# Optimization experiments

Hardware: AMD Instinct MI355X
Metric: run time of the kernel (lower is better)

The kernel has to match this reference:

```python
import jax, jax.numpy as jnp
import numpy as np
from jax import lax

B, C_IN, H, W = 16, 64, 64, 64
C_OUT, K, P, NC = 128, 3, 1, 512
PS = C_IN * K * K  # 576 patch feature size


def setup_inputs() -> dict:
    key = jax.random.key(0)
    k0, k1, k2, k3 = jax.random.split(key, 4)
    x = jax.random.normal(k0, (B, C_IN, H, W), jnp.float32)
    cluster_centers = jax.random.normal(k1, (NC, PS), jnp.float32)
    temp = jnp.ones((1,), jnp.float32)
    weight = jax.random.normal(k2, (C_OUT, C_IN, K, K), jnp.float32) * 0.05
    bias = jax.random.normal(k3, (C_OUT,), jnp.float32) * 0.05
    return {"x": x, "cluster_centers": cluster_centers, "temp": temp,
            "weight": weight, "bias": bias}


def _forward(x, cluster_centers, temp, weight, bias):
    Bx, C, Hx, Wx = x.shape
    t = temp.reshape(())  # scalar temperature
    # F.unfold: patches ordered (c, kh, kw) along feature dim -> [B, C*K*K, H, W]
    patches = lax.conv_general_dilated_patches(
        x, (K, K), (1, 1), padding=((P, P), (P, P)))
    L = Hx * Wx  # number of blocks; equals Wx*Wx (H==W, same-padding, stride 1)
    cols = patches.reshape(Bx, PS, L)               # this_patch
    flat = cols.transpose(0, 2, 1).reshape(-1, PS)  # [N, PS] flat_patches
    # torch.cdist (p=2): stable squared-distance expansion, single GEMM
    d2 = (jnp.sum(flat * flat, axis=1, keepdims=True)
          + jnp.sum(cluster_centers * cluster_centers, axis=1)[None, :]
          - 2.0 * (flat @ cluster_centers.T))
    dist = jnp.sqrt(jnp.maximum(d2, 0.0))           # [N, NC]
    soft = jax.nn.softmax(-dist * t, axis=1)        # soft assignments
    transformed = soft @ cluster_centers            # [N, PS]
    final = (t * transformed + flat) / (t + 1.0)
    # Faithful to the original's view_as: raw reshape WITHOUT transposing back
    final = final.reshape(Bx, PS, L)
    # F.fold(output_size=(W*K, W*K), kernel=K, padding=P, stride=K):
    # non-overlapping tiles on padded canvas, then crop P from each side.
    # (b, c, kh, kw, bh, bw) -> (b, c, bh, kh, bw, kw)
    tile = (final.reshape(Bx, C, K, K, Wx, Wx)
                 .transpose(0, 1, 4, 2, 5, 3)
                 .reshape(Bx, C, Wx * K, Wx * K))
    # crop offset P=1 at the top/left; bottom/right of cropped region is zero
    x_refold = jnp.pad(tile[:, :, P:, P:], ((0, 0), (0, 0), (0, P), (0, P)))
    # F.conv2d(..., stride=kernel_size, padding=padding)
    out = lax.conv_general_dilated(
        x_refold, weight, window_strides=(K, K), padding=((P, P), (P, P)),
        dimension_numbers=("NCHW", "OIHW", "NCHW"))
    return out + bias[None, :, None, None]


def reference(x, cluster_centers, temp, weight, bias):
    return _forward(x, cluster_centers, temp, weight, bias)
```

## Files before the change

kernel.cpp:

```cpp
#include <hip/hip_runtime.h>
#include <stdint.h>

typedef __bf16 bf16;
typedef bf16 bf16x2 __attribute__((ext_vector_type(2)));
typedef bf16 bf16x8 __attribute__((ext_vector_type(8)));
typedef float f32x4 __attribute__((ext_vector_type(4)));

static constexpr int B_    = 16;
static constexpr int C_IN  = 64;
static constexpr int H_    = 64;
static constexpr int W_    = 64;
static constexpr int C_OUT = 128;
static constexpr int NC    = 512;
static constexpr int PS    = 576;
static constexpr int L_    = H_ * W_;
static constexpr int NR    = B_ * L_;

#define DEVI __device__ __forceinline__

DEVI void gload_lds16(const void* g, void* l) {
  __builtin_amdgcn_global_load_lds(
      (const __attribute__((address_space(1))) uint32_t*)g,
      (__attribute__((address_space(3))) uint32_t*)l, 16, 0, 0);
}


__global__ void prep_w_kernel(const float* __restrict__ w, bf16* __restrict__ WB,
                              bf16* __restrict__ ccT) {
  int i = blockIdx.x * 256 + threadIdx.x;
  if (i < C_OUT * PS) WB[i] = (bf16)w[i];
  if (i < 64 * NC) ccT[(size_t)PS * NC + i] = (bf16)0.f;
}

__global__ void prep_cc_kernel(const float* __restrict__ cc, bf16* __restrict__ ccB,
                               bf16* __restrict__ ccT, float* __restrict__ cn) {
  int j = blockIdx.x;
  const float* src = cc + (size_t)j * PS;
  float s = 0.f;
  for (int p = threadIdx.x; p < PS; p += 256) {
    float v = src[p];
    bf16 bv = (bf16)v;
    ccB[(size_t)j * PS + p] = bv;
    ccT[(size_t)p * NC + j] = bv;
    float fv = (float)bv;
    s += fv * fv;
  }
  for (int o = 32; o; o >>= 1) s += __shfl_xor(s, o);
  __shared__ float red[4];
  int lane = threadIdx.x & 63, wid = threadIdx.x >> 6;
  if (lane == 0) red[wid] = s;
  __syncthreads();
  if (threadIdx.x == 0) cn[j] = red[0] + red[1] + red[2] + red[3];
}

static constexpr int XS_STRIDE = 66;
static constexpr int XS_PLANE  = 64 * XS_STRIDE;
static constexpr int XS_OFF    = 2;

__global__ void __launch_bounds__(256, 4) patch_kernel(
    const float* __restrict__ x, bf16* __restrict__ flatB,
    float* __restrict__ rn, float* __restrict__ rsum) {
  __shared__ bf16 xs[XS_OFF + 3 * XS_PLANE + 64];
  const int bh = blockIdx.x;
  const int b = bh >> 6, h = bh & 63;
  const size_t bOff = (size_t)b * (C_IN * L_);
#pragma unroll
  for (int it = 0; it < 12; ++it) {
    int idx = threadIdx.x + it * 256;
    int plane = idx >> 10;
    int rem = idx & 1023;
    int c = rem >> 4;
    int f4 = rem & 15;
    int y = h + plane - 1;
    int e = XS_OFF + plane * XS_PLANE + c * XS_STRIDE + f4 * 4;
    bf16x2 lo = {(bf16)0.f, (bf16)0.f}, hi = {(bf16)0.f, (bf16)0.f};
    if ((unsigned)y < 64u) {
      float4 v = *(const float4*)(x + bOff + (size_t)c * L_ + y * 64 + f4 * 4);
      lo = bf16x2{(bf16)v.x, (bf16)v.y};
      hi = bf16x2{(bf16)v.z, (bf16)v.w};
    }
    *(bf16x2*)(xs + e) = lo;
    *(bf16x2*)(xs + e + 2) = hi;
  }
  __syncthreads();

  const int lane = threadIdx.x & 63, wid = threadIdx.x >> 6;
  int eb[8], km[8];
#pragma unroll
  for (int q = 0; q < 8; q++) {
    int p = lane * 8 + q;
    int c = p / 9, r9 = p - c * 9;
    int kh = r9 / 3, kw = r9 - kh * 3;
    eb[q] = kh * XS_PLANE + c * XS_STRIDE + (kw - 1);
    km[q] = kw - 1;
  }
  int ebt[8], kmt[8];
  {
    int pl = (lane & 7) * 8;
#pragma unroll
    for (int q = 0; q < 8; q++) {
      int p = 512 + pl + q;
      int c = p / 9, r9 = p - c * 9;
      int kh = r9 / 3, kw = r9 - kh * 3;
      ebt[q] = kh * XS_PLANE + c * XS_STRIDE + (kw - 1);
      kmt[q] = kw - 1;
    }
  }
  for (int it = 0; it < 16; ++it) {
    int w = wid * 16 + it;
    int row = bh * 64 + w;
    bf16* outp = flatB + (size_t)row * PS;
    float s = 0.f;
    bf16x8 v;
#pragma unroll
    for (int q = 0; q < 8; q++) {
      int xx = w + km[q];
      float fv = ((unsigned)xx < 64u) ? (float)xs[XS_OFF + eb[q] + w] : 0.f;
      v[q] = (bf16)fv;
      s += fv * fv;
    }
    *(bf16x8*)(outp + lane * 8) = v;
    if (lane < 8) {
      bf16x8 v2;
#pragma unroll
      for (int q = 0; q < 8; q++) {
        int xx = w + kmt[q];
        float fv = ((unsigned)xx < 64u) ? (float)xs[XS_OFF + ebt[q] + w] : 0.f;
        v2[q] = (bf16)fv;
        s += fv * fv;
      }
      *(bf16x8*)(outp + 512 + lane * 8) = v2;
    }
    for (int o = 32; o; o >>= 1) s += __shfl_xor(s, o);
    if (lane == 0) { rn[row] = s; rsum[row] = 0.f; }
  }
}

template <int EPI, int GX>
__global__ void __launch_bounds__(256, 5) gemm_nt(
    const bf16* __restrict__ A, int lda, const bf16* __restrict__ Bm, int ldb,
    int M, int N, int Kd,
    const float* __restrict__ e0, const float* __restrict__ e1,
    const float* __restrict__ e2, const bf16* flatB,
    float* outF, bf16* outB, int ldc) {
  const int blk = blockIdx.x;
  const int xcd = blk & 7;
  const int k = blk >> 3;
  const int ypx = (gridDim.x >> 3) / GX;
  const int bx = k % GX;
  const int by = xcd * ypx + k / GX;
  const int m0 = by * 128, n0 = bx * 64;

  __shared__ bf16 As[128 * 64];
  __shared__ bf16 Bs[64 * 64];
  const int tid = threadIdx.x;
  const int lane = tid & 63;
  const int wid = tid >> 6;
  const int wr = wid >> 1, wc = wid & 1;

  const int srow = tid >> 3;
  const int sch = ((tid & 7) ^ (srow & 7)) * 8;
  const bf16* gA = A + (size_t)(m0 + srow) * lda + sch;
  const bf16* gB = Bm + (size_t)(n0 + srow) * ldb + sch;
  bf16* lA = As + tid * 8;
  bf16* lB = Bs + tid * 8;

  const int lrow = lane & 15;
  const int kq = lane >> 4;
  const int axor = lrow & 7;
  const int arow = (wr * 64 + lrow) * 64;
  const int brow = (wc * 32 + lrow) * 64;

  f32x4 acc[4][2];
#pragma unroll
  for (int i = 0; i < 4; i++)
#pragma unroll
    for (int j = 0; j < 2; j++) acc[i][j] = f32x4{0.f, 0.f, 0.f, 0.f};

  const int nk = Kd >> 6;
  for (int kt = 0; kt < nk; ++kt) {
    __syncthreads();
    const bf16* ga = gA + kt * 64;
    const bf16* gb = gB + kt * 64;
#pragma unroll
    for (int q = 0; q < 4; ++q)
      gload_lds16(ga + (size_t)(q * 32) * lda, lA + q * 2048);
#pragma unroll
    for (int q = 0; q < 2; ++q)
      gload_lds16(gb + (size_t)(q * 32) * ldb, lB + q * 2048);
    __syncthreads();
#pragma unroll
    for (int h = 0; h < 2; ++h) {
      const int cs = ((h * 4 + kq) ^ axor) * 8;
      bf16x8 af[4], bfr[2];
#pragma unroll
      for (int i = 0; i < 4; i++) af[i] = *(const bf16x8*)(As + arow + i * 1024 + cs);
#pragma unroll
      for (int j = 0; j < 2; j++) bfr[j] = *(const bf16x8*)(Bs + brow + j * 1024 + cs);
#pragma unroll
      for (int i = 0; i < 4; i++)
#pragma unroll
        for (int j = 0; j < 2; j++)
          acc[i][j] = __builtin_amdgcn_mfma_f32_16x16x32_bf16(af[i], bfr[j], acc[i][j], 0, 0, 0);
    }
  }

  const int rb = m0 + wr * 64 + kq * 4;
  const int cb = n0 + wc * 32 + lrow;
  if constexpr (EPI == 1) {
    float t = e2[0];
#pragma unroll
    for (int i = 0; i < 4; i++) {
      float rowsum[4] = {0.f, 0.f, 0.f, 0.f};
#pragma unroll
      for (int j = 0; j < 2; j++) {
        int col = cb + j * 16;
        float cnv = e1[col];
#pragma unroll
        for (int r = 0; r < 4; r++) {
          int row = rb + i * 16 + r;
          float d2 = e0[row] + cnv - 2.f * acc[i][j][r];
          float e = __expf(-t * sqrtf(fmaxf(d2, 0.f)));
          outB[(size_t)row * ldc + col] = (bf16)e;
          rowsum[r] += e;
        }
      }
#pragma unroll
      for (int r = 0; r < 4; r++) {
        float s = rowsum[r];
        s += __shfl_xor(s, 1);
        s += __shfl_xor(s, 2);
        s += __shfl_xor(s, 4);
        s += __shfl_xor(s, 8);
        if (lrow == 0) atomicAdd(outF + rb + i * 16 + r, s);
      }
    }
  } else {
    float t = e0[0];
    float inv = 1.f / (t + 1.f);
#pragma unroll
    for (int i = 0; i < 4; i++) {
      float arw[4];
#pragma unroll
      for (int r = 0; r < 4; r++) arw[r] = t * inv / e1[rb + i * 16 + r];
#pragma unroll
      for (int j = 0; j < 2; j++) {
        int col = cb + j * 16;
#pragma unroll
        for (int r = 0; r < 4; r++) {
          int row = rb + i * 16 + r;
          float fl = (float)flatB[(size_t)row * PS + col];
          float v = acc[i][j][r] * arw[r] + fl * inv;
          outB[(size_t)row * ldc + col] = (bf16)v;
        }
      }
    }
  }
}

__global__ void __launch_bounds__(256, 4) gemm3_kernel(
    const bf16* __restrict__ A, const bf16* __restrict__ F,
    const float* __restrict__ bias, float* __restrict__ outF) {
  const size_t bz = blockIdx.z;
  const bf16* Fb = F + bz * (size_t)L_ * PS;
  float* outp = outF + bz * (size_t)C_OUT * L_;
  const int n0 = blockIdx.x * 128;

  __shared__ bf16 As[128 * 64];
  __shared__ bf16 Bs[128 * 64];
  const int tid = threadIdx.x;
  const int lane = tid & 63;
  const int wid = tid >> 6;
  const int wr = wid >> 1, wc = wid & 1;

  const int srow = tid >> 3;
  const int sch = ((tid & 7) ^ (srow & 7)) * 8;
  const bf16* gA = A + (size_t)srow * PS + sch;
  bf16* lA = As + tid * 8;

  const int lrow = lane & 15;
  const int kq = lane >> 4;
  const int axor = lrow & 7;
  const int arow = (wr * 64 + lrow) * 64;
  const int brow = (wc * 64 + lrow) * 64;

  f32x4 acc[4][4];
#pragma unroll
  for (int i = 0; i < 4; i++)
#pragma unroll
    for (int j = 0; j < 4; j++) acc[i][j] = f32x4{0.f, 0.f, 0.f, 0.f};

  const int nk = PS / 64;
  for (int kt = 0; kt < nk; ++kt) {
    __syncthreads();
    const bf16* ga = gA + kt * 64;
#pragma unroll
    for (int q = 0; q < 4; ++q)
      gload_lds16(ga + (size_t)(q * 32) * PS, lA + q * 2048);
#pragma unroll
    for (int ps = 0; ps < 2; ++ps) {
      int id = tid + ps * 256;
      int pp = id >> 4;
      int lc = id & 15;
      int pl = 2 * pp;
      int pg = kt * 64 + pl;
      const bf16* s0 = Fb + (size_t)pg * L_ + n0 + lc * 8;
      bf16x8 v0 = *(const bf16x8*)s0;
      bf16x8 v1 = *(const bf16x8*)(s0 + L_);
      int l8 = n0 + lc * 8;
      int oh = l8 >> 6;
      bool ow0 = (l8 & 63) == 0;
      int r90 = pg % 9;
      int kh0 = r90 / 3, kw0 = r90 - 3 * kh0;
      int r91 = (pg + 1) % 9;
      int kh1 = r91 / 3, kw1 = r91 - 3 * kh1;
      if (oh == 0 && kh0 == 0) {
#pragma unroll
        for (int e = 0; e < 8; e++) v0[e] = (bf16)0.f;
      }
      if (ow0 && kw0 == 0) v0[0] = (bf16)0.f;
      if (oh == 0 && kh1 == 0) {
#pragma unroll
        for (int e = 0; e < 8; e++) v1[e] = (bf16)0.f;
      }
      if (ow0 && kw1 == 0) v1[0] = (bf16)0.f;
#pragma unroll
      for (int e = 0; e < 8; ++e) {
        int l = lc * 8 + e;
        int addr = l * 64 + (((pl >> 3) ^ (l & 7)) << 3) + (pl & 7);
        *(bf16x2*)(Bs + addr) = bf16x2{v0[e], v1[e]};
      }
    }
    __syncthreads();
#pragma unroll
    for (int h = 0; h < 2; ++h) {
      const int cs = ((h * 4 + kq) ^ axor) * 8;
      bf16x8 af[4], bfr[4];
#pragma unroll
      for (int i = 0; i < 4; i++) af[i] = *(const bf16x8*)(As + arow + i * 1024 + cs);
#pragma unroll
      for (int j = 0; j < 4; j++) bfr[j] = *(const bf16x8*)(Bs + brow + j * 1024 + cs);
#pragma unroll
      for (int i = 0; i < 4; i++)
#pragma unroll
        for (int j = 0; j < 4; j++)
          acc[i][j] = __builtin_amdgcn_mfma_f32_16x16x32_bf16(af[i], bfr[j], acc[i][j], 0, 0, 0);
    }
  }

  const int rb = wr * 64 + kq * 4;
  const int cb = n0 + wc * 64 + lrow;
#pragma unroll
  for (int i = 0; i < 4; i++) {
#pragma unroll
    for (int j = 0; j < 4; j++) {
      int col = cb + j * 16;
#pragma unroll
      for (int r = 0; r < 4; r++) {
        int row = rb + i * 16 + r;
        outp[(size_t)row * L_ + col] = acc[i][j][r] + bias[row];
      }
    }
  }
}


extern "C" void kernel_launch(void* const* d_in, const int* in_sizes, int n_in,
                              void* d_out, int out_size, void* d_ws, size_t ws_size,
                              hipStream_t stream) {
  (void)in_sizes; (void)n_in; (void)out_size; (void)ws_size;
  const float* x    = (const float*)d_in[0];
  const float* cc   = (const float*)d_in[1];
  const float* tp   = (const float*)d_in[2];
  const float* w    = (const float*)d_in[3];
  const float* bias = (const float*)d_in[4];
  float* out = (float*)d_out;

  char* ws = (char*)d_ws;
  size_t off = 0;
  auto alloc = [&](size_t bytes) {
    char* p = ws + off;
    off += (bytes + 255) & ~(size_t)255;
    return p;
  };
  bf16* ccB   = (bf16*)alloc((size_t)NC * PS * 2);
  bf16* ccT   = (bf16*)alloc((size_t)640 * NC * 2);
  float* cn   = (float*)alloc((size_t)NC * 4);
  bf16* WB    = (bf16*)alloc((size_t)C_OUT * PS * 2);
  float* rn   = (float*)alloc((size_t)NR * 4);
  float* rsum = (float*)alloc((size_t)NR * 4);
  bf16* flatB = (bf16*)alloc((size_t)NR * PS * 2);
  bf16* E     = (bf16*)alloc((size_t)NR * NC * 2);

  prep_w_kernel<<<dim3(288), dim3(256), 0, stream>>>(w, WB, ccT);
  prep_cc_kernel<<<dim3(NC), dim3(256), 0, stream>>>(cc, ccB, ccT, cn);
  patch_kernel<<<dim3(B_ * H_), dim3(256), 0, stream>>>(x, flatB, rn, rsum);
  gemm_nt<1, 8><<<dim3((NR / 128) * (NC / 64)), dim3(256), 0, stream>>>(
      flatB, PS, ccB, PS, NR, NC, PS, rn, cn, tp, nullptr, rsum, E, NC);
  gemm_nt<2, 9><<<dim3((NR / 128) * (PS / 64)), dim3(256), 0, stream>>>(
      E, NC, ccT, NC, NR, PS, NC, tp, rsum, nullptr, flatB, nullptr, flatB, PS);
  gemm3_kernel<<<dim3(L_ / 128, 1, B_), dim3(256), 0, stream>>>(WB, flatB, bias, out);
}
```

Baseline: 246.6 us.

## Widen gemm_nt tiles to 128x128 and switch to 32x32x16 MFMA

The two middle GEMMs now use 128x128 output tiles instead of 128x64, so each warp covers a 64x64 sub-tile with 32x32x16 bf16 MFMA instructions in place of 16x16x32. This reuses each A tile across twice as many columns and cuts the number of LDS fragment reads per MFMA, lowering global and LDS traffic per FLOP. The second GEMM (N=576) uses 5 column tiles with a bounds check, padded by the existing 640-row ccT buffer, so some compute is wasted. Epilogues are rewritten for the 32x32 accumulator layout, and launch bounds drop to 4 waves/SIMD to allow more registers.

```diff
diff --git a/kernel.cpp b/kernel.cpp
--- a/kernel.cpp
+++ b/kernel.cpp
@@ -5,6 +5,7 @@
 typedef bf16 bf16x2 __attribute__((ext_vector_type(2)));
 typedef bf16 bf16x8 __attribute__((ext_vector_type(8)));
 typedef float f32x4 __attribute__((ext_vector_type(4)));
+typedef float f32x16 __attribute__((ext_vector_type(16)));
 
 static constexpr int B_    = 16;
 static constexpr int C_IN  = 64;
@@ -137,7 +138,7 @@
 }
 
 template <int EPI, int GX>
-__global__ void __launch_bounds__(256, 5) gemm_nt(
+__global__ void __launch_bounds__(256, 4) gemm_nt(
     const bf16* __restrict__ A, int lda, const bf16* __restrict__ Bm, int ldb,
     int M, int N, int Kd,
     const float* __restrict__ e0, const float* __restrict__ e1,
@@ -149,10 +150,10 @@
   const int ypx = (gridDim.x >> 3) / GX;
   const int bx = k % GX;
   const int by = xcd * ypx + k / GX;
-  const int m0 = by * 128, n0 = bx * 64;
+  const int m0 = by * 128, n0 = bx * 128;
 
   __shared__ bf16 As[128 * 64];
-  __shared__ bf16 Bs[64 * 64];
+  __shared__ bf16 Bs[128 * 64];
   const int tid = threadIdx.x;
   const int lane = tid & 63;
   const int wid = tid >> 6;
@@ -165,17 +166,19 @@
   bf16* lA = As + tid * 8;
   bf16* lB = Bs + tid * 8;
 
-  const int lrow = lane & 15;
-  const int kq = lane >> 4;
-  const int axor = lrow & 7;
-  const int arow = (wr * 64 + lrow) * 64;
-  const int brow = (wc * 32 + lrow) * 64;
-
-  f32x4 acc[4][2];
-#pragma unroll
-  for (int i = 0; i < 4; i++)
-#pragma unroll
-    for (int j = 0; j < 2; j++) acc[i][j] = f32x4{0.f, 0.f, 0.f, 0.f};
+  const int l31 = lane & 31;
+  const int khalf = lane >> 5;
+  const int arow0 = (wr * 64 + l31) * 64;
+  const int brow0 = (wc * 64 + l31) * 64;
+  const int axor0 = l31 & 7;
+
+  f32x16 acc[2][2];
+#pragma unroll
+  for (int i = 0; i < 2; i++)
+#pragma unroll
+    for (int j = 0; j < 2; j++)
+#pragma unroll
+      for (int r = 0; r < 16; r++) acc[i][j][r] = 0.f;
 
   const int nk = Kd >> 6;
   for (int kt = 0; kt < nk; ++kt) {
@@ -183,75 +186,79 @@
     const bf16* ga = gA + kt * 64;
     const bf16* gb = gB + kt * 64;
 #pragma unroll
-    for (int q = 0; q < 4; ++q)
+    for (int q = 0; q < 4; ++q) {
       gload_lds16(ga + (size_t)(q * 32) * lda, lA + q * 2048);
-#pragma unroll
-    for (int q = 0; q < 2; ++q)
       gload_lds16(gb + (size_t)(q * 32) * ldb, lB + q * 2048);
+    }
     __syncthreads();
 #pragma unroll
-    for (int h = 0; h < 2; ++h) {
-      const int cs = ((h * 4 + kq) ^ axor) * 8;
-      bf16x8 af[4], bfr[2];
-#pragma unroll
-      for (int i = 0; i < 4; i++) af[i] = *(const bf16x8*)(As + arow + i * 1024 + cs);
-#pragma unroll
-      for (int j = 0; j < 2; j++) bfr[j] = *(const bf16x8*)(Bs + brow + j * 1024 + cs);
-#pragma unroll
-      for (int i = 0; i < 4; i++)
+    for (int s = 0; s < 4; ++s) {
+      const int chunk = 2 * s + khalf;
+      bf16x8 af[2], bf[2];
+#pragma unroll
+      for (int i = 0; i < 2; i++) {
+        int row = wr * 64 + i * 32 + l31;
+        af[i] = *(const bf16x8*)(As + arow0 + i * 2048 + ((chunk ^ (row & 7)) * 8));
+      }
+#pragma unroll
+      for (int j = 0; j < 2; j++) {
+        int row = wc * 64 + j * 32 + l31;
+        bf[j] = *(const bf16x8*)(Bs + brow0 + j * 2048 + ((chunk ^ (row & 7)) * 8));
+      }
+#pragma unroll
+      for (int i = 0; i < 2; i++)
 #pragma unroll
         for (int j = 0; j < 2; j++)
-          acc[i][j] = __builtin_amdgcn_mfma_f32_16x16x32_bf16(af[i], bfr[j], acc[i][j], 0, 0, 0);
-    }
-  }
-
-  const int rb = m0 + wr * 64 + kq * 4;
-  const int cb = n0 + wc * 32 + lrow;
+          acc[i][j] = __builtin_amdgcn_mfma_f32_32x32x16_bf16(af[i], bf[j], acc[i][j], 0, 0, 0);
+    }
+  }
+
+  const int rbase = m0 + wr * 64 + 4 * khalf;
+  const int cbase = n0 + wc * 64 + l31;
   if constexpr (EPI == 1) {
     float t = e2[0];
-#pragma unroll
-    for (int i = 0; i < 4; i++) {
-      float rowsum[4] = {0.f, 0.f, 0.f, 0.f};
-#pragma unroll
-      for (int j = 0; j < 2; j++) {
-        int col = cb + j * 16;
-        float cnv = e1[col];
-#pragma unroll
-        for (int r = 0; r < 4; r++) {
-          int row = rb + i * 16 + r;
-          float d2 = e0[row] + cnv - 2.f * acc[i][j][r];
+    float cnv[2];
+#pragma unroll
+    for (int j = 0; j < 2; j++) cnv[j] = e1[cbase + j * 32];
+#pragma unroll
+    for (int i = 0; i < 2; i++) {
+#pragma unroll
+      for (int rg = 0; rg < 16; rg++) {
+        int row = rbase + i * 32 + (rg & 3) + 8 * (rg >> 2);
+        float rnv = e0[row];
+        float es = 0.f;
+#pragma unroll
+        for (int j = 0; j < 2; j++) {
+          float d2 = rnv + cnv[j] - 2.f * acc[i][j][rg];
           float e = __expf(-t * sqrtf(fmaxf(d2, 0.f)));
-          outB[(size_t)row * ldc + col] = (bf16)e;
-          rowsum[r] += e;
+          outB[(size_t)row * ldc + cbase + j * 32] = (bf16)e;
+          es += e;
         }
-      }
-#pragma unroll
-      for (int r = 0; r < 4; r++) {
-        float s = rowsum[r];
-        s += __shfl_xor(s, 1);
-        s += __shfl_xor(s, 2);
-        s += __shfl_xor(s, 4);
-        s += __shfl_xor(s, 8);
-        if (lrow == 0) atomicAdd(outF + rb + i * 16 + r, s);
+        es += __shfl_xor(es, 1);
+        es += __shfl_xor(es, 2);
+        es += __shfl_xor(es, 4);
+        es += __shfl_xor(es, 8);
+        es += __shfl_xor(es, 16);
+        if (l31 == 0) atomicAdd(outF + row, es);
       }
     }
   } else {
     float t = e0[0];
     float inv = 1.f / (t + 1.f);
 #pragma unroll
-    for (int i = 0; i < 4; i++) {
-      float arw[4];
-#pragma unroll
-      for (int r = 0; r < 4; r++) arw[r] = t * inv / e1[rb + i * 16 + r];
-#pragma unroll
-      for (int j = 0; j < 2; j++) {
-        int col = cb + j * 16;
-#pragma unroll
-        for (int r = 0; r < 4; r++) {
-          int row = rb + i * 16 + r;
-          float fl = (float)flatB[(size_t)row * PS + col];
-          float v = acc[i][j][r] * arw[r] + fl * inv;
-          outB[(size_t)row * ldc + col] = (bf16)v;
+    for (int i = 0; i < 2; i++) {
+#pragma unroll
+      for (int rg = 0; rg < 16; rg++) {
+        int row = rbase + i * 32 + (rg & 3) + 8 * (rg >> 2);
+        float arw = t * inv / e1[row];
+#pragma unroll
+        for (int j = 0; j < 2; j++) {
+          int col = cbase + j * 32;
+          if (col < N) {
+            float fl = (float)flatB[(size_t)row * PS + col];
+            float v = acc[i][j][rg] * arw + fl * inv;
+            outB[(size_t)row * ldc + col] = (bf16)v;
+          }
         }
       }
     }
@@ -395,9 +402,9 @@
   prep_w_kernel<<<dim3(288), dim3(256), 0, stream>>>(w, WB, ccT);
   prep_cc_kernel<<<dim3(NC), dim3(256), 0, stream>>>(cc, ccB, ccT, cn);
   patch_kernel<<<dim3(B_ * H_), dim3(256), 0, stream>>>(x, flatB, rn, rsum);
-  gemm_nt<1, 8><<<dim3((NR / 128) * (NC / 64)), dim3(256), 0, stream>>>(
+  gemm_nt<1, 4><<<dim3((NC / 128) * (NR / 128)), dim3(256), 0, stream>>>(
       flatB, PS, ccB, PS, NR, NC, PS, rn, cn, tp, nullptr, rsum, E, NC);
-  gemm_nt<2, 9><<<dim3((NR / 128) * (PS / 64)), dim3(256), 0, stream>>>(
+  gemm_nt<2, 5><<<dim3(5 * (NR / 128)), dim3(256), 0, stream>>>(
       E, NC, ccT, NC, NR, PS, NC, tp, rsum, nullptr, flatB, nullptr, flatB, PS);
   gemm3_kernel<<<dim3(L_ / 128, 1, B_), dim3(256), 0, stream>>>(WB, flatB, bias, out);
 }
```

After: 289.9 us. 17.6% more time.
